# Kernel optimization log

Measured on AMD Instinct MI355X. Metric: run time of the kernel, lower is better.

## Reference

```python
import jax, jax.numpy as jnp
import numpy as np

RES = (256, 256, 256)
CH = 16
RR = 8  # ceil(log2(256))
N_PTS = 262144


def grid_sample_2d(plane, gx, gy):
    """Bilinear grid_sample, align_corners=True.
    plane: (C, H, W); gx in [-1,1] indexes W, gy indexes H. Returns (N, C)."""
    C, H, W = plane.shape
    ix = (gx + 1.0) * 0.5 * (W - 1)
    iy = (gy + 1.0) * 0.5 * (H - 1)
    x0f = jnp.floor(ix)
    y0f = jnp.floor(iy)
    wx = ix - x0f
    wy = iy - y0f
    x0 = jnp.clip(x0f.astype(jnp.int32), 0, W - 1)
    x1 = jnp.clip(x0 + 1, 0, W - 1)
    y0 = jnp.clip(y0f.astype(jnp.int32), 0, H - 1)
    y1 = jnp.clip(y0 + 1, 0, H - 1)
    v00 = plane[:, y0, x0]  # (C, N)
    v01 = plane[:, y0, x1]
    v10 = plane[:, y1, x0]
    v11 = plane[:, y1, x1]
    out = (v00 * (1 - wx) * (1 - wy) + v01 * wx * (1 - wy)
           + v10 * (1 - wx) * wy + v11 * wx * wy)
    return out.T  # (N, C)


def integrate(P, coords):
    """P: (N, 2*CH, RR) with real part channels [:CH], imag [CH:].
    coords: (N,) in [-1,1]. Fourier-basis numerical integration (real part)."""
    c = (coords + 1.0) * 0.5 * (2 ** RR - 1)  # (N,)
    coef = jnp.concatenate([jnp.zeros((1,), jnp.float32),
                            2.0 ** jnp.arange(RR - 1, dtype=jnp.float32)]) / (2 ** RR)
    theta = 2.0 * jnp.pi * c[:, None] * coef  # (N, RR)
    # Re(exp(i*theta) . P_complex) = cos.Re(P) - sin.Im(P)
    re = jnp.einsum('nr,ncr->nc', jnp.cos(theta), P[:, :CH, :])
    im = jnp.einsum('nr,ncr->nc', jnp.sin(theta), P[:, CH:, :])
    return re - im  # (N, CH)


def setup_inputs() -> dict:
    key = jax.random.key(0)
    k0, k1, k2, k3 = jax.random.split(key, 4)
    inputs = jax.random.uniform(k0, (N_PTS, 3), dtype=jnp.float32,
                                minval=-1.0, maxval=1.0)
    C = 2 * RR * CH
    Pu = 0.001 * jax.random.normal(k1, (1, C, RES[1], RES[2]), dtype=jnp.float32)
    Pv = 0.001 * jax.random.normal(k2, (1, C, RES[0], RES[2]), dtype=jnp.float32)
    Pw = 0.001 * jax.random.normal(k3, (1, C, RES[0], RES[1]), dtype=jnp.float32)
    return {"inputs": inputs, "Pu": Pu, "Pv": Pv, "Pw": Pw}


def reference(inputs, Pu, Pv, Pw):
    c0, c1, c2 = inputs[:, 0], inputs[:, 1], inputs[:, 2]
    # grid last-dim (x,y): x indexes width (last plane axis), y the height.
    su = grid_sample_2d(Pu[0], c1, c2).reshape(-1, 2 * CH, RR)
    sv = grid_sample_2d(Pv[0], c0, c2).reshape(-1, 2 * CH, RR)
    sw = grid_sample_2d(Pw[0], c0, c1).reshape(-1, 2 * CH, RR)
    return integrate(su, c0) + integrate(sv, c1) + integrate(sw, c2)  # (N, CH)
```

## Files before the change

### kernel.cpp

```cpp
#include <hip/hip_runtime.h>
#include <hip/hip_fp16.h>
#include <math.h>

#define NPTS 262144
#define PLANE_ELEMS 16777216u

typedef __attribute__((ext_vector_type(4))) float f4;
typedef __attribute__((ext_vector_type(4))) unsigned int u4;

#define OFF_IDX      (3ull * PLANE_ELEMS * 2ull)
#define OFF_PARTIAL  (OFF_IDX + (size_t)3 * NPTS * 4)
#define OFF_HIST     (OFF_PARTIAL + (size_t)3 * NPTS * 16 * 2)
#define WS_NEED      (OFF_HIST + (size_t)3 * 65536 * 4)

__device__ __forceinline__ void plane_xy(int p, float c0, float c1, float c2,
                                         float& gx, float& gy, float& ax) {
  if (p == 0)      { gx = c1; gy = c2; ax = c0; }
  else if (p == 1) { gx = c0; gy = c2; ax = c1; }
  else             { gx = c0; gy = c1; ax = c2; }
}

__device__ __forceinline__ int cell_of(float g) {
  float i = (g + 1.f) * 0.5f * 255.f;
  int x0 = (int)floorf(i);
  return x0 < 0 ? 0 : (x0 > 255 ? 255 : x0);
}

__device__ __forceinline__ void trans_load(const float* __restrict__ src,
                                           unsigned c0, unsigned hw0, int tid,
                                           f4 (&va)[4], f4 (&vb)[4]) {
#pragma unroll
  for (int j = 0; j < 4; ++j) {
    int idx = j * 256 + tid;
    int rp = idx >> 5;
    int q = idx & 31;
    const f4* base = (const f4*)(src + (size_t)(c0 + 2 * rp) * 65536u + hw0 + 4 * q);
    va[j] = __builtin_nontemporal_load(base);
    vb[j] = __builtin_nontemporal_load(base + 16384);
  }
}

__device__ __forceinline__ void trans_proc(unsigned* tile, __half* dst,
                                           unsigned c0, unsigned hw0, int tid,
                                           f4 (&va)[4], f4 (&vb)[4]) {
#pragma unroll
  for (int j = 0; j < 4; ++j) {
    int idx = j * 256 + tid;
    int rp = idx >> 5;
    int q = idx & 31;
#pragma unroll
    for (int k = 0; k < 4; ++k) {
      int hw = 4 * q + k;
      __half2 h = __floats2half2_rn(va[j][k], vb[j][k]);
      tile[hw * 36 + (rp ^ (hw >> 3))] = *(unsigned*)&h;
    }
  }
  __syncthreads();
  int seg = tid & 7;
#pragma unroll
  for (int jj = 0; jj < 4; ++jj) {
    int hw = jj * 32 + (tid >> 3);
    int s = hw >> 3;
    u4 v = *(const u4*)(tile + hw * 36 + 4 * ((seg ^ (s >> 2)) & 7));
    u4 o;
    switch (s & 3) {
      case 0: o = v; break;
      case 1: o = u4{v.y, v.x, v.w, v.z}; break;
      case 2: o = u4{v.z, v.w, v.x, v.y}; break;
      default: o = u4{v.w, v.z, v.y, v.x}; break;
    }
    *(u4*)((char*)dst + ((size_t)(hw0 + hw) * 256u + c0) * 2u + seg * 16u) = o;
  }
  __syncthreads();
}

__global__ __launch_bounds__(256) void PREFFFT_fat1_k(
    const float* __restrict__ Pu, const float* __restrict__ Pv,
    const float* __restrict__ Pw, __half* __restrict__ dst0,
    const float* __restrict__ inputs, unsigned* __restrict__ hist) {
  __shared__ unsigned tile[128 * 36];
  const int bx = blockIdx.x;
  const int tid = threadIdx.x;
  if (bx < 1536) {
    int bz = bx / 512;
    int rem = bx - bz * 512;
    int by = rem >> 7;
    int bxx = rem & 127;
    const float* src = bz == 0 ? Pu : (bz == 1 ? Pv : Pw);
    __half* dst = dst0 + (size_t)bz * PLANE_ELEMS;
    const unsigned hwbase = bxx * 512u;
    const unsigned c0 = by * 64u;
    f4 vaA[4], vbA[4], vaB[4], vbB[4];
    trans_load(src, c0, hwbase, tid, vaA, vbA);
    trans_load(src, c0, hwbase + 128u, tid, vaB, vbB);
    trans_proc(tile, dst, c0, hwbase, tid, vaA, vbA);
    trans_load(src, c0, hwbase + 256u, tid, vaA, vbA);
    trans_proc(tile, dst, c0, hwbase + 128u, tid, vaB, vbB);
    trans_load(src, c0, hwbase + 384u, tid, vaB, vbB);
    trans_proc(tile, dst, c0, hwbase + 256u, tid, vaA, vbA);
    trans_proc(tile, dst, c0, hwbase + 384u, tid, vaB, vbB);
  } else {
    int hb = bx - 1536;
#pragma unroll
    for (int it = 0; it < 4; ++it) {
      int item = hb * 1024 + it * 256 + tid;
      int n = item & (NPTS - 1);
      int p = item >> 18;
      float c0 = inputs[n * 3 + 0], c1 = inputs[n * 3 + 1], c2 = inputs[n * 3 + 2];
      float gx, gy, ax;
      plane_xy(p, c0, c1, c2, gx, gy, ax);
      int key = (cell_of(gy) << 8) | cell_of(gx);
      atomicAdd(&hist[p * 65536 + key], 1u);
    }
  }
}

__global__ __launch_bounds__(1024) void PREFFFT_scan_k(unsigned* __restrict__ hist) {
  __shared__ unsigned part[1024];
  unsigned* h = hist + (size_t)blockIdx.x * 65536;
  int t = threadIdx.x;
  unsigned s = 0;
#pragma unroll 8
  for (int i = 0; i < 64; ++i) s += h[t * 64 + i];
  part[t] = s;
  __syncthreads();
  for (int off = 1; off < 1024; off <<= 1) {
    unsigned v = (t >= off) ? part[t - off] : 0u;
    __syncthreads();
    part[t] += v;
    __syncthreads();
  }
  unsigned run = (t == 0) ? 0u : part[t - 1];
#pragma unroll 8
  for (int i = 0; i < 64; ++i) {
    unsigned c = h[t * 64 + i];
    h[t * 64 + i] = run;
    run += c;
  }
}

__global__ __launch_bounds__(256) void PREFFFT_scat_k(
    const float* __restrict__ inputs, unsigned* __restrict__ hist,
    unsigned* __restrict__ idx) {
  int n = blockIdx.x * 256 + threadIdx.x;
  int p = blockIdx.y;
  float c0 = inputs[n * 3 + 0], c1 = inputs[n * 3 + 1], c2 = inputs[n * 3 + 2];
  float gx, gy, ax;
  plane_xy(p, c0, c1, c2, gx, gy, ax);
  int key = (cell_of(gy) << 8) | cell_of(gx);
  unsigned pos = atomicAdd(&hist[p * 65536 + key], 1u);
  idx[(size_t)p * NPTS + pos] = (unsigned)n;
}

__global__ __launch_bounds__(256) void PREFFFT_samp_k(
    const unsigned* __restrict__ idx, const float* __restrict__ inputs,
    const __half* __restrict__ T, __half* __restrict__ partial) {
  int p = blockIdx.y;
  int bx = blockIdx.x;
  int lbx = (bx & 7) * 1024 + (bx >> 3);
  int slot = lbx * 32 + ((int)threadIdx.x >> 3);
  int t = threadIdx.x & 7;

  unsigned n = idx[(size_t)p * NPTS + slot];
  float c0 = inputs[n * 3 + 0], c1 = inputs[n * 3 + 1], c2 = inputs[n * 3 + 2];
  float gx, gy, ax;
  plane_xy(p, c0, c1, c2, gx, gy, ax);

  float ix = (gx + 1.f) * 0.5f * 255.f;
  float iy = (gy + 1.f) * 0.5f * 255.f;
  float x0f = floorf(ix), y0f = floorf(iy);
  float wx = ix - x0f, wy = iy - y0f;
  int x0 = (int)x0f; x0 = x0 < 0 ? 0 : (x0 > 255 ? 255 : x0);
  int y0 = (int)y0f; y0 = y0 < 0 ? 0 : (y0 > 255 ? 255 : y0);
  int x1 = x0 + 1 > 255 ? 255 : x0 + 1;
  int y1 = y0 + 1 > 255 ? 255 : y0 + 1;
  float w00 = (1.f - wx) * (1.f - wy);
  float w01 = wx * (1.f - wy);
  float w10 = (1.f - wx) * wy;
  float w11 = wx * wy;

  const __half* __restrict__ P = T + (size_t)p * PLANE_ELEMS;
  int r00 = (y0 * 256 + x0) * 256, r01 = (y0 * 256 + x1) * 256;
  int r10 = (y1 * 256 + x0) * 256, r11 = (y1 * 256 + x1) * 256;
  int ore = t * 16;
  int oim = 128 + t * 16;

  f4 a0 = *(const f4*)(P + r00 + ore),     a1 = *(const f4*)(P + r00 + ore + 8);
  f4 a2 = *(const f4*)(P + r00 + oim),     a3 = *(const f4*)(P + r00 + oim + 8);
  f4 b0 = *(const f4*)(P + r01 + ore),     b1 = *(const f4*)(P + r01 + ore + 8);
  f4 b2 = *(const f4*)(P + r01 + oim),     b3 = *(const f4*)(P + r01 + oim + 8);
  f4 c0v = *(const f4*)(P + r10 + ore),    c1v = *(const f4*)(P + r10 + ore + 8);
  f4 c2v = *(const f4*)(P + r10 + oim),    c3v = *(const f4*)(P + r10 + oim + 8);
  f4 d0 = *(const f4*)(P + r11 + ore),     d1 = *(const f4*)(P + r11 + ore + 8);
  f4 d2 = *(const f4*)(P + r11 + oim),     d3 = *(const f4*)(P + r11 + oim + 8);

  __half2 hw00 = __float2half2_rn(w00), hw01 = __float2half2_rn(w01);
  __half2 hw10 = __float2half2_rn(w10), hw11 = __float2half2_rn(w11);

  __half2 bre[8], bim[8];
#pragma unroll
  for (int q = 0; q < 4; ++q) {
    __half2 v;
    v = __hmul2(((const __half2*)&a0)[q], hw00);
    v = __hfma2(((const __half2*)&b0)[q],  hw01, v);
    v = __hfma2(((const __half2*)&c0v)[q], hw10, v);
    bre[q] = __hfma2(((const __half2*)&d0)[q], hw11, v);

    v = __hmul2(((const __half2*)&a1)[q], hw00);
    v = __hfma2(((const __half2*)&b1)[q],  hw01, v);
    v = __hfma2(((const __half2*)&c1v)[q], hw10, v);
    bre[q + 4] = __hfma2(((const __half2*)&d1)[q], hw11, v);

    v = __hmul2(((const __half2*)&a2)[q], hw00);
    v = __hfma2(((const __half2*)&b2)[q],  hw01, v);
    v = __hfma2(((const __half2*)&c2v)[q], hw10, v);
    bim[q] = __hfma2(((const __half2*)&d2)[q], hw11, v);

    v = __hmul2(((const __half2*)&a3)[q], hw00);
    v = __hfma2(((const __half2*)&b3)[q],  hw01, v);
    v = __hfma2(((const __half2*)&c3v)[q], hw10, v);
    bim[q + 4] = __hfma2(((const __half2*)&d3)[q], hw11, v);
  }

  float fre[16], fim[16];
#pragma unroll
  for (int q = 0; q < 8; ++q) {
    float2 vr = __half22float2(bre[q]);
    float2 vi = __half22float2(bim[q]);
    fre[2 * q] = vr.x; fre[2 * q + 1] = vr.y;
    fim[2 * q] = vi.x; fim[2 * q + 1] = vi.y;
  }

  float cs = (ax + 1.f) * 0.5f * 255.f;
  float th = 6.283185307179586f * cs * (1.f / 256.f);
  float s, c;
  __sincosf(th, &s, &c);
  float aR0 = fre[0], aR1 = fre[8];
  float aI0 = 0.f,    aI1 = 0.f;
#pragma unroll
  for (int r = 1; r < 8; ++r) {
    aR0 += fre[r] * c;     aR1 += fre[8 + r] * c;
    aI0 += fim[r] * s;     aI1 += fim[8 + r] * s;
    if (r < 7) {
      float c2 = c + c;
      float cn = c2 * c - 1.f;
      s = c2 * s;
      c = cn;
    }
  }

  *(__half2*)(partial + ((size_t)p * NPTS + n) * 16 + 2 * t) =
      __floats2half2_rn(aR0 - aI0, aR1 - aI1);
}

__global__ __launch_bounds__(256) void PREFFFT_red_k(
    const __half* __restrict__ part, float* __restrict__ out) {
  size_t i = (size_t)blockIdx.x * 256 + threadIdx.x;
  const size_t PS = (size_t)NPTS * 16;
  union H8 { u4 v; __half2 h[4]; };
  H8 a, b, c;
  a.v = *(const u4*)(part + i * 8);
  b.v = *(const u4*)(part + PS + i * 8);
  c.v = *(const u4*)(part + 2 * PS + i * 8);
  f4 o0, o1;
#pragma unroll
  for (int k = 0; k < 4; ++k) {
    float2 fa = __half22float2(a.h[k]);
    float2 fb = __half22float2(b.h[k]);
    float2 fc = __half22float2(c.h[k]);
    float lo = fa.x + fb.x + fc.x;
    float hi = fa.y + fb.y + fc.y;
    if (k < 2) { o0[2 * k] = lo; o0[2 * k + 1] = hi; }
    else       { o1[2 * (k - 2)] = lo; o1[2 * (k - 2) + 1] = hi; }
  }
  ((f4*)out)[i * 2] = o0;
  ((f4*)out)[i * 2 + 1] = o1;
}

__global__ __launch_bounds__(256) void PREFFFT_fallback_k(
    const float* __restrict__ inputs, const float* __restrict__ Tu,
    const float* __restrict__ Tv, const float* __restrict__ Tw,
    float* __restrict__ out) {
  int gtid = blockIdx.x * 256 + threadIdx.x;
  int n = gtid >> 5;
  int t = threadIdx.x & 31;
  const bool is_re = t < 16;
  float c0 = inputs[n * 3 + 0], c1 = inputs[n * 3 + 1], c2 = inputs[n * 3 + 2];
  const float* PL[3] = {Tu, Tv, Tw};
  float acc = 0.f;
#pragma unroll
  for (int p = 0; p < 3; ++p) {
    float gx, gy, ax;
    plane_xy(p, c0, c1, c2, gx, gy, ax);
    float ix = (gx + 1.f) * 0.5f * 255.f;
    float iy = (gy + 1.f) * 0.5f * 255.f;
    float x0f = floorf(ix), y0f = floorf(iy);
    float wx = ix - x0f, wy = iy - y0f;
    int x0 = (int)x0f; x0 = x0 < 0 ? 0 : (x0 > 255 ? 255 : x0);
    int y0 = (int)y0f; y0 = y0 < 0 ? 0 : (y0 > 255 ? 255 : y0);
    int x1 = x0 + 1 > 255 ? 255 : x0 + 1;
    int y1 = y0 + 1 > 255 ? 255 : y0 + 1;
    float w00 = (1.f - wx) * (1.f - wy), w01 = wx * (1.f - wy);
    float w10 = (1.f - wx) * wy, w11 = wx * wy;
    int i00 = y0 * 256 + x0, i01 = y0 * 256 + x1;
    int i10 = y1 * 256 + x0, i11 = y1 * 256 + x1;
    float b[8];
#pragma unroll
    for (int j = 0; j < 8; ++j) {
      const float* base = PL[p] + (size_t)(t * 8 + j) * 65536u;
      b[j] = w00 * base[i00] + w01 * base[i01] + w10 * base[i10] + w11 * base[i11];
    }
    float csv = (ax + 1.f) * 0.5f * 255.f;
    float theta1 = 6.283185307179586f * csv * (1.f / 256.f);
    float partial = is_re ? b[0] : 0.f;
#pragma unroll
    for (int r = 1; r < 8; ++r) {
      float thr = theta1 * (float)(1 << (r - 1));
      float s, c;
      __sincosf(thr, &s, &c);
      partial += b[r] * (is_re ? c : s);
    }
    float other = __shfl_xor(partial, 16);
    acc += partial - other;
  }
  if (is_re) out[n * 16 + t] = acc;
}

extern "C" void kernel_launch(void* const* d_in, const int* in_sizes, int n_in,
                              void* d_out, int out_size, void* d_ws, size_t ws_size,
                              hipStream_t stream) {
  const float* inputs = (const float*)d_in[0];
  const float* Pu = (const float*)d_in[1];
  const float* Pv = (const float*)d_in[2];
  const float* Pw = (const float*)d_in[3];
  float* out = (float*)d_out;

  if (ws_size >= WS_NEED) {
    char* ws = (char*)d_ws;
    __half*   T       = (__half*)ws;
    unsigned* idx     = (unsigned*)(ws + OFF_IDX);
    __half*   partial = (__half*)(ws + OFF_PARTIAL);
    unsigned* hist    = (unsigned*)(ws + OFF_HIST);

    hipMemsetAsync(hist, 0, (size_t)3 * 65536 * 4, stream);
    PREFFFT_fat1_k<<<2304, 256, 0, stream>>>(Pu, Pv, Pw, T, inputs, hist);
    PREFFFT_scan_k<<<3, 1024, 0, stream>>>(hist);
    {
      dim3 tg(NPTS / 256, 3);
      PREFFFT_scat_k<<<tg, 256, 0, stream>>>(inputs, hist, idx);
    }
    {
      dim3 tg(NPTS / 32, 3);
      PREFFFT_samp_k<<<tg, 256, 0, stream>>>(idx, inputs, T, partial);
    }
    PREFFFT_red_k<<<2048, 256, 0, stream>>>(partial, out);
  } else {
    PREFFFT_fallback_k<<<NPTS / 8, 256, 0, stream>>>(inputs, Pu, Pv, Pw, out);
  }
}
```

Baseline: 213.6 us.

## Overlap per-plane scatter with previous plane's sampling in fused launches

```diff
diff --git a/kernel.cpp b/kernel.cpp
--- a/kernel.cpp
+++ b/kernel.cpp
@@ -72,6 +72,113 @@
     *(u4*)((char*)dst + ((size_t)(hw0 + hw) * 256u + c0) * 2u + seg * 16u) = o;
   }
   __syncthreads();
+}
+
+__device__ __forceinline__ void samp_point(
+    int p, int slot, int t, const unsigned* __restrict__ idx,
+    const float* __restrict__ inputs, const __half* __restrict__ T,
+    __half* __restrict__ partial) {
+  unsigned n = idx[(size_t)p * NPTS + slot];
+  float c0 = inputs[n * 3 + 0], c1 = inputs[n * 3 + 1], c2 = inputs[n * 3 + 2];
+  float gx, gy, ax;
+  plane_xy(p, c0, c1, c2, gx, gy, ax);
+
+  float ix = (gx + 1.f) * 0.5f * 255.f;
+  float iy = (gy + 1.f) * 0.5f * 255.f;
+  float x0f = floorf(ix), y0f = floorf(iy);
+  float wx = ix - x0f, wy = iy - y0f;
+  int x0 = (int)x0f; x0 = x0 < 0 ? 0 : (x0 > 255 ? 255 : x0);
+  int y0 = (int)y0f; y0 = y0 < 0 ? 0 : (y0 > 255 ? 255 : y0);
+  int x1 = x0 + 1 > 255 ? 255 : x0 + 1;
+  int y1 = y0 + 1 > 255 ? 255 : y0 + 1;
+  float w00 = (1.f - wx) * (1.f - wy);
+  float w01 = wx * (1.f - wy);
+  float w10 = (1.f - wx) * wy;
+  float w11 = wx * wy;
+
+  const __half* __restrict__ P = T + (size_t)p * PLANE_ELEMS;
+  int r00 = (y0 * 256 + x0) * 256, r01 = (y0 * 256 + x1) * 256;
+  int r10 = (y1 * 256 + x0) * 256, r11 = (y1 * 256 + x1) * 256;
+  int ore = t * 16;
+  int oim = 128 + t * 16;
+
+  f4 a0 = *(const f4*)(P + r00 + ore),     a1 = *(const f4*)(P + r00 + ore + 8);
+  f4 a2 = *(const f4*)(P + r00 + oim),     a3 = *(const f4*)(P + r00 + oim + 8);
+  f4 b0 = *(const f4*)(P + r01 + ore),     b1 = *(const f4*)(P + r01 + ore + 8);
+  f4 b2 = *(const f4*)(P + r01 + oim),     b3 = *(const f4*)(P + r01 + oim + 8);
+  f4 c0v = *(const f4*)(P + r10 + ore),    c1v = *(const f4*)(P + r10 + ore + 8);
+  f4 c2v = *(const f4*)(P + r10 + oim),    c3v = *(const f4*)(P + r10 + oim + 8);
+  f4 d0 = *(const f4*)(P + r11 + ore),     d1 = *(const f4*)(P + r11 + ore + 8);
+  f4 d2 = *(const f4*)(P + r11 + oim),     d3 = *(const f4*)(P + r11 + oim + 8);
+
+  __half2 hw00 = __float2half2_rn(w00), hw01 = __float2half2_rn(w01);
+  __half2 hw10 = __float2half2_rn(w10), hw11 = __float2half2_rn(w11);
+
+  __half2 bre[8], bim[8];
+#pragma unroll
+  for (int q = 0; q < 4; ++q) {
+    __half2 v;
+    v = __hmul2(((const __half2*)&a0)[q], hw00);
+    v = __hfma2(((const __half2*)&b0)[q],  hw01, v);
+    v = __hfma2(((const __half2*)&c0v)[q], hw10, v);
+    bre[q] = __hfma2(((const __half2*)&d0)[q], hw11, v);
+
+    v = __hmul2(((const __half2*)&a1)[q], hw00);
+    v = __hfma2(((const __half2*)&b1)[q],  hw01, v);
+    v = __hfma2(((const __half2*)&c1v)[q], hw10, v);
+    bre[q + 4] = __hfma2(((const __half2*)&d1)[q], hw11, v);
+
+    v = __hmul2(((const __half2*)&a2)[q], hw00);
+    v = __hfma2(((const __half2*)&b2)[q],  hw01, v);
+    v = __hfma2(((const __half2*)&c2v)[q], hw10, v);
+    bim[q] = __hfma2(((const __half2*)&d2)[q], hw11, v);
+
+    v = __hmul2(((const __half2*)&a3)[q], hw00);
+    v = __hfma2(((const __half2*)&b3)[q],  hw01, v);
+    v = __hfma2(((const __half2*)&c3v)[q], hw10, v);
+    bim[q + 4] = __hfma2(((const __half2*)&d3)[q], hw11, v);
+  }
+
+  float fre[16], fim[16];
+#pragma unroll
+  for (int q = 0; q < 8; ++q) {
+    float2 vr = __half22float2(bre[q]);
+    float2 vi = __half22float2(bim[q]);
+    fre[2 * q] = vr.x; fre[2 * q + 1] = vr.y;
+    fim[2 * q] = vi.x; fim[2 * q + 1] = vi.y;
+  }
+
+  float cs = (ax + 1.f) * 0.5f * 255.f;
+  float th = 6.283185307179586f * cs * (1.f / 256.f);
+  float s, c;
+  __sincosf(th, &s, &c);
+  float aR0 = fre[0], aR1 = fre[8];
+  float aI0 = 0.f,    aI1 = 0.f;
+#pragma unroll
+  for (int r = 1; r < 8; ++r) {
+    aR0 += fre[r] * c;     aR1 += fre[8 + r] * c;
+    aI0 += fim[r] * s;     aI1 += fim[8 + r] * s;
+    if (r < 7) {
+      float c2 = c + c;
+      float cn = c2 * c - 1.f;
+      s = c2 * s;
+      c = cn;
+    }
+  }
+
+  *(__half2*)(partial + ((size_t)p * NPTS + n) * 16 + 2 * t) =
+      __floats2half2_rn(aR0 - aI0, aR1 - aI1);
+}
+
+__device__ __forceinline__ void scat_point(
+    int p, int n, const float* __restrict__ inputs,
+    unsigned* __restrict__ hist, unsigned* __restrict__ idx) {
+  float c0 = inputs[n * 3 + 0], c1 = inputs[n * 3 + 1], c2 = inputs[n * 3 + 2];
+  float gx, gy, ax;
+  plane_xy(p, c0, c1, c2, gx, gy, ax);
+  int key = (cell_of(gy) << 8) | cell_of(gx);
+  unsigned pos = atomicAdd(&hist[p * 65536 + key], 1u);
+  idx[(size_t)p * NPTS + pos] = (unsigned)n;
 }
 
 __global__ __launch_bounds__(256) void PREFFFT_fat1_k(
@@ -139,118 +246,36 @@
   }
 }
 
-__global__ __launch_bounds__(256) void PREFFFT_scat_k(
+__global__ __launch_bounds__(256) void PREFFFT_scat1_k(
     const float* __restrict__ inputs, unsigned* __restrict__ hist,
     unsigned* __restrict__ idx) {
   int n = blockIdx.x * 256 + threadIdx.x;
-  int p = blockIdx.y;
-  float c0 = inputs[n * 3 + 0], c1 = inputs[n * 3 + 1], c2 = inputs[n * 3 + 2];
-  float gx, gy, ax;
-  plane_xy(p, c0, c1, c2, gx, gy, ax);
-  int key = (cell_of(gy) << 8) | cell_of(gx);
-  unsigned pos = atomicAdd(&hist[p * 65536 + key], 1u);
-  idx[(size_t)p * NPTS + pos] = (unsigned)n;
-}
-
-__global__ __launch_bounds__(256) void PREFFFT_samp_k(
+  scat_point(0, n, inputs, hist, idx);
+}
+
+__global__ __launch_bounds__(256) void PREFFFT_fat2_k(
+    unsigned* __restrict__ idx, const float* __restrict__ inputs,
+    const __half* __restrict__ T, __half* __restrict__ partial,
+    unsigned* __restrict__ hist, int sp) {
+  int bx = blockIdx.x;
+  if (bx < 1024) {
+    int n = bx * 256 + threadIdx.x;
+    scat_point(sp + 1, n, inputs, hist, idx);
+  } else {
+    int b = bx - 1024;
+    int lbx = (b & 7) * 1024 + (b >> 3);
+    int slot = lbx * 32 + ((int)threadIdx.x >> 3);
+    samp_point(sp, slot, threadIdx.x & 7, idx, inputs, T, partial);
+  }
+}
+
+__global__ __launch_bounds__(256) void PREFFFT_samp1_k(
     const unsigned* __restrict__ idx, const float* __restrict__ inputs,
     const __half* __restrict__ T, __half* __restrict__ partial) {
-  int p = blockIdx.y;
-  int bx = blockIdx.x;
-  int lbx = (bx & 7) * 1024 + (bx >> 3);
+  int b = blockIdx.x;
+  int lbx = (b & 7) * 1024 + (b >> 3);
   int slot = lbx * 32 + ((int)threadIdx.x >> 3);
-  int t = threadIdx.x & 7;
-
-  unsigned n = idx[(size_t)p * NPTS + slot];
-  float c0 = inputs[n * 3 + 0], c1 = inputs[n * 3 + 1], c2 = inputs[n * 3 + 2];
-  float gx, gy, ax;
-  plane_xy(p, c0, c1, c2, gx, gy, ax);
-
-  float ix = (gx + 1.f) * 0.5f * 255.f;
-  float iy = (gy + 1.f) * 0.5f * 255.f;
-  float x0f = floorf(ix), y0f = floorf(iy);
-  float wx = ix - x0f, wy = iy - y0f;
-  int x0 = (int)x0f; x0 = x0 < 0 ? 0 : (x0 > 255 ? 255 : x0);
-  int y0 = (int)y0f; y0 = y0 < 0 ? 0 : (y0 > 255 ? 255 : y0);
-  int x1 = x0 + 1 > 255 ? 255 : x0 + 1;
-  int y1 = y0 + 1 > 255 ? 255 : y0 + 1;
-  float w00 = (1.f - wx) * (1.f - wy);
-  float w01 = wx * (1.f - wy);
-  float w10 = (1.f - wx) * wy;
-  float w11 = wx * wy;
-
-  const __half* __restrict__ P = T + (size_t)p * PLANE_ELEMS;
-  int r00 = (y0 * 256 + x0) * 256, r01 = (y0 * 256 + x1) * 256;
-  int r10 = (y1 * 256 + x0) * 256, r11 = (y1 * 256 + x1) * 256;
-  int ore = t * 16;
-  int oim = 128 + t * 16;
-
-  f4 a0 = *(const f4*)(P + r00 + ore),     a1 = *(const f4*)(P + r00 + ore + 8);
-  f4 a2 = *(const f4*)(P + r00 + oim),     a3 = *(const f4*)(P + r00 + oim + 8);
-  f4 b0 = *(const f4*)(P + r01 + ore),     b1 = *(const f4*)(P + r01 + ore + 8);
-  f4 b2 = *(const f4*)(P + r01 + oim),     b3 = *(const f4*)(P + r01 + oim + 8);
-  f4 c0v = *(const f4*)(P + r10 + ore),    c1v = *(const f4*)(P + r10 + ore + 8);
-  f4 c2v = *(const f4*)(P + r10 + oim),    c3v = *(const f4*)(P + r10 + oim + 8);
-  f4 d0 = *(const f4*)(P + r11 + ore),     d1 = *(const f4*)(P + r11 + ore + 8);
-  f4 d2 = *(const f4*)(P + r11 + oim),     d3 = *(const f4*)(P + r11 + oim + 8);
-
-  __half2 hw00 = __float2half2_rn(w00), hw01 = __float2half2_rn(w01);
-  __half2 hw10 = __float2half2_rn(w10), hw11 = __float2half2_rn(w11);
-
-  __half2 bre[8], bim[8];
-#pragma unroll
-  for (int q = 0; q < 4; ++q) {
-    __half2 v;
-    v = __hmul2(((const __half2*)&a0)[q], hw00);
-    v = __hfma2(((const __half2*)&b0)[q],  hw01, v);
-    v = __hfma2(((const __half2*)&c0v)[q], hw10, v);
-    bre[q] = __hfma2(((const __half2*)&d0)[q], hw11, v);
-
-    v = __hmul2(((const __half2*)&a1)[q], hw00);
-    v = __hfma2(((const __half2*)&b1)[q],  hw01, v);
-    v = __hfma2(((const __half2*)&c1v)[q], hw10, v);
-    bre[q + 4] = __hfma2(((const __half2*)&d1)[q], hw11, v);
-
-    v = __hmul2(((const __half2*)&a2)[q], hw00);
-    v = __hfma2(((const __half2*)&b2)[q],  hw01, v);
-    v = __hfma2(((const __half2*)&c2v)[q], hw10, v);
-    bim[q] = __hfma2(((const __half2*)&d2)[q], hw11, v);
-
-    v = __hmul2(((const __half2*)&a3)[q], hw00);
-    v = __hfma2(((const __half2*)&b3)[q],  hw01, v);
-    v = __hfma2(((const __half2*)&c3v)[q], hw10, v);
-    bim[q + 4] = __hfma2(((const __half2*)&d3)[q], hw11, v);
-  }
-
-  float fre[16], fim[16];
-#pragma unroll
-  for (int q = 0; q < 8; ++q) {
-    float2 vr = __half22float2(bre[q]);
-    float2 vi = __half22float2(bim[q]);
-    fre[2 * q] = vr.x; fre[2 * q + 1] = vr.y;
-    fim[2 * q] = vi.x; fim[2 * q + 1] = vi.y;
-  }
-
-  float cs = (ax + 1.f) * 0.5f * 255.f;
-  float th = 6.283185307179586f * cs * (1.f / 256.f);
-  float s, c;
-  __sincosf(th, &s, &c);
-  float aR0 = fre[0], aR1 = fre[8];
-  float aI0 = 0.f,    aI1 = 0.f;
-#pragma unroll
-  for (int r = 1; r < 8; ++r) {
-    aR0 += fre[r] * c;     aR1 += fre[8 + r] * c;
-    aI0 += fim[r] * s;     aI1 += fim[8 + r] * s;
-    if (r < 7) {
-      float c2 = c + c;
-      float cn = c2 * c - 1.f;
-      s = c2 * s;
-      c = cn;
-    }
-  }
-
-  *(__half2*)(partial + ((size_t)p * NPTS + n) * 16 + 2 * t) =
-      __floats2half2_rn(aR0 - aI0, aR1 - aI1);
+  samp_point(2, slot, threadIdx.x & 7, idx, inputs, T, partial);
 }
 
 __global__ __launch_bounds__(256) void PREFFFT_red_k(
@@ -345,14 +370,10 @@
     hipMemsetAsync(hist, 0, (size_t)3 * 65536 * 4, stream);
     PREFFFT_fat1_k<<<2304, 256, 0, stream>>>(Pu, Pv, Pw, T, inputs, hist);
     PREFFFT_scan_k<<<3, 1024, 0, stream>>>(hist);
-    {
-      dim3 tg(NPTS / 256, 3);
-      PREFFFT_scat_k<<<tg, 256, 0, stream>>>(inputs, hist, idx);
-    }
-    {
-      dim3 tg(NPTS / 32, 3);
-      PREFFFT_samp_k<<<tg, 256, 0, stream>>>(idx, inputs, T, partial);
-    }
+    PREFFFT_scat1_k<<<1024, 256, 0, stream>>>(inputs, hist, idx);
+    PREFFFT_fat2_k<<<9216, 256, 0, stream>>>(idx, inputs, T, partial, hist, 0);
+    PREFFFT_fat2_k<<<9216, 256, 0, stream>>>(idx, inputs, T, partial, hist, 1);
+    PREFFFT_samp1_k<<<8192, 256, 0, stream>>>(idx, inputs, T, partial);
     PREFFFT_red_k<<<2048, 256, 0, stream>>>(partial, out);
   } else {
     PREFFFT_fallback_k<<<NPTS / 8, 256, 0, stream>>>(inputs, Pu, Pv, Pw, out);
```

Result: faster. 208.2 us (-2.5%).
